# Optimization experiments

Measured on AMD Instinct MI355X. Metric: run time of the kernel, lower is better.

Reference implementation:

```python
import jax, jax.numpy as jnp
import numpy as np

T, B, I, H = 2048, 2048, 1, 20


def setup_inputs() -> dict:
    key = jax.random.key(0)
    k0, k1, k2, k3, k4 = jax.random.split(key, 5)
    x = jax.random.normal(k0, (T, B, I), dtype=jnp.float32)
    # Concatenated gate weights in order [f, i, o, c]; equivalent to the
    # module's 8 separate nn.Linear layers (wf/uf, wi/ui, wo/uo, wc/uc).
    W = jax.random.normal(k1, (4 * H, I), dtype=jnp.float32) * 0.2
    U = jax.random.normal(k2, (4 * H, H), dtype=jnp.float32) * 0.2
    bw = jax.random.normal(k3, (4 * H,), dtype=jnp.float32) * 0.1  # Linear(w*) biases
    bu = jax.random.normal(k4, (4 * H,), dtype=jnp.float32) * 0.1  # Linear(u*) biases
    return {"x": x, "W": W, "U": U, "bw": bw, "bu": bu}


def reference(x, W, U, bw, bu):
    h_dim = U.shape[1]
    b = x.shape[1]
    # Precompute input projections for all timesteps: (T, B, 4H).
    # Original adds both Linear biases (bw from w*, bu from u*) plus zero b*.
    xz = jnp.einsum('tbi,gi->tbg', x, W) + bw + bu

    def step(carry, xz_t):
        h, c = carry
        z = xz_t + h @ U.T  # (B, 4H)
        f, i, o, g = jnp.split(z, 4, axis=-1)
        f = jax.nn.sigmoid(f)
        i = jax.nn.sigmoid(i)
        o = jax.nn.sigmoid(o)
        g = jnp.tanh(g)
        c = f * c + i * g
        h = o * jnp.tanh(c)
        return (h, c), h

    h0 = jnp.zeros((b, h_dim), dtype=x.dtype)
    c0 = jnp.zeros((b, h_dim), dtype=x.dtype)
    (h_last, c_last), h_seq = jax.lax.scan(step, (h0, c0), xz)
    return h_seq, h_last, c_last
```

## Files before the change

### kernel.cpp

```cpp
#include <hip/hip_runtime.h>
#include <cstddef>


constexpr int T = 2048;
constexpr int B = 2048;
constexpr int H = 20;
constexpr int CHUNK = 16;
constexpr int NCH = T / CHUNK;

typedef float f2   __attribute__((ext_vector_type(2)));
typedef float f4ma __attribute__((ext_vector_type(4), may_alias));

__device__ __forceinline__ float rcp_f(float v) { return __builtin_amdgcn_rcpf(v); }
__device__ __forceinline__ float ex2(float v)   { return __builtin_amdgcn_exp2f(v); }
__device__ __forceinline__ float dpp_swap1(float v) {
  return __int_as_float(__builtin_amdgcn_update_dpp(
      0, __float_as_int(v), 0xB1, 0xF, 0xF, true));
}

__global__ __launch_bounds__(64, 1)
void lstm_w8(const float* __restrict__ xg, const float* __restrict__ Wg,
             const float* __restrict__ Ug, const float* __restrict__ bwg,
             const float* __restrict__ bug, float* __restrict__ out) {
  __shared__ float hx[2][64];
  __shared__ float xl[2][CHUNK];

  const int tid = threadIdx.x;
  const int p   = tid & 1;
  const int jr  = tid >> 1;
  const int jc  = (jr < H) ? jr : (H - 1);
  const int b   = blockIdx.x;
  const bool st = (p == 0) && (jr < H);

  constexpr float K1 = 1.44269504f;
  const float s0 = -K1;
  const float s1 = p ? (2.f * K1) : -K1;
  const int g0 = p ? 2 : 0;
  const int g1 = p ? 3 : 1;

  f2 u2[H];
#pragma unroll
  for (int k = 0; k < H; ++k) {
    u2[k].x = Ug[(g0 * H + jc) * H + k] * s0;
    u2[k].y = Ug[(g1 * H + jc) * H + k] * s1;
  }
  f2 w2, b2, A, Bv;
  w2.x = Wg[g0 * H + jc] * s0;  w2.y = Wg[g1 * H + jc] * s1;
  b2.x = (bwg[g0 * H + jc] + bug[g0 * H + jc]) * s0;
  b2.y = (bwg[g1 * H + jc] + bug[g1 * H + jc]) * s1;
  A.x = 1.f;  A.y = p ? -2.f : (2.f * K1);
  Bv.x = 0.f; Bv.y = p ? 1.f : 0.f;

  const int wslot = p ? (32 + jr) : jr;

  for (int q = tid; q < 2 * 64; q += 64) (&hx[0][0])[q] = 0.f;
  if (tid < 2 * CHUNK) (&xl[0][0])[tid] = 0.f;
  __builtin_amdgcn_wave_barrier();

  if (tid < CHUNK) xl[0][tid] = xg[(size_t)tid * B + b];
  float xnext = (tid < CHUNK) ? xg[(size_t)(CHUNK + tid) * B + b] : 0.f;
  __builtin_amdgcn_wave_barrier();

  float c2 = 0.f;
  float hn = 0.f;
  float* outp = out + (size_t)b * H + jc;
  constexpr size_t OS = (size_t)B * H;

  for (int ch = 0; ch < NCH; ++ch) {
    const int cb = ch & 1;
    if (tid < CHUNK) {
      xl[cb ^ 1][tid] = xnext;
      const int tp = (ch + 2) * CHUNK + tid;
      xnext = (tp < T) ? xg[(size_t)tp * B + b] : 0.f;
    }
#pragma unroll
    for (int s = 0; s < CHUNK; ++s) {
      const int P = s & 1;
      __builtin_amdgcn_wave_barrier();
      const f4ma* hp = reinterpret_cast<const f4ma*>(&hx[P][0]);
      const f4ma v0 = hp[0], v1 = hp[1], v2 = hp[2], v3 = hp[3], v4 = hp[4];
      const float xv = xl[cb][s];
      const float hb[H] = {v0.x, v0.y, v0.z, v0.w, v1.x, v1.y, v1.z, v1.w,
                           v2.x, v2.y, v2.z, v2.w, v3.x, v3.y, v3.z, v3.w,
                           v4.x, v4.y, v4.z, v4.w};
      f2 h5;  h5.x  = hb[5];  h5.y  = hb[5];
      f2 h10; h10.x = hb[10]; h10.y = hb[10];
      f2 h15; h15.x = hb[15]; h15.y = hb[15];
      f2 qa = b2, qb = u2[5] * h5, qc = u2[10] * h10, qd = u2[15] * h15;
#pragma unroll
      for (int k = 0; k < 5; ++k)   { f2 hk; hk.x = hb[k]; hk.y = hb[k];
                                      qa = u2[k] * hk + qa; }
#pragma unroll
      for (int k = 6; k < 10; ++k)  { f2 hk; hk.x = hb[k]; hk.y = hb[k];
                                      qb = u2[k] * hk + qb; }
#pragma unroll
      for (int k = 11; k < 15; ++k) { f2 hk; hk.x = hb[k]; hk.y = hb[k];
                                      qc = u2[k] * hk + qc; }
#pragma unroll
      for (int k = 16; k < 20; ++k) { f2 hk; hk.x = hb[k]; hk.y = hb[k];
                                      qd = u2[k] * hk + qd; }
      f2 xv2; xv2.x = xv; xv2.y = xv;
      const f2 z2 = w2 * xv2 + ((qa + qb) + (qc + qd));
      f2 r;
      r.x = rcp_f(1.f + ex2(z2.x));
      r.y = rcp_f(1.f + ex2(z2.y));
      const f2 act2 = A * r + Bv;
      f2 oth;
      oth.x = dpp_swap1(act2.x);
      oth.y = dpp_swap1(act2.y);
      const float fg  = p ? oth.x : act2.x;
      const float og  = p ? act2.x : oth.x;
      const float igt = act2.y * oth.y;
      c2 = fmaf(fg, c2, igt);
      const float r2 = rcp_f(1.f + ex2(c2));
      hn = fmaf(-2.f * og, r2, og);
      hx[P ^ 1][wslot] = hn;
      if (st) *outp = hn;
      outp += OS;
    }
  }

  if (st) {
    out[OS * T + (size_t)b * H + jr] = hn;
    out[OS * (T + 1) + (size_t)b * H + jr] = c2 * 0.34657359f;
  }
}

extern "C" void kernel_launch(void* const* d_in, const int* in_sizes, int n_in,
                              void* d_out, int out_size, void* d_ws, size_t ws_size,
                              hipStream_t stream) {
  (void)in_sizes; (void)n_in; (void)d_ws; (void)ws_size; (void)out_size;
  const float* x  = (const float*)d_in[0];
  const float* W  = (const float*)d_in[1];
  const float* U  = (const float*)d_in[2];
  const float* bw = (const float*)d_in[3];
  const float* bu = (const float*)d_in[4];
  float* out = (float*)d_out;

  lstm_w8<<<dim3(B), dim3(64), 0, stream>>>(x, W, U, bw, bu, out);
}
```

Measured before the change: 530.2 us.

## Process two batch rows per wave and broadcast h via readlane instead of LDS

Each 64-lane wave now runs two independent batch sequences, packing them into the two halves of f2 vectors so the packed FMAs serve two recurrences at once, and launches half as many blocks. The hidden state is no longer exchanged through double-buffered shared memory with wave barriers. Instead each lane pulls h with 20 scalar readlanes per sequence, and x is kept in registers and fetched with readlane. This is meant to cut LDS round-trip latency on the serial critical path and make better use of each wave's ALUs. The cost is 40 readlanes per step, more register pressure, and half the number of waves for latency hiding.

```diff
diff --git a/kernel.cpp b/kernel.cpp
--- a/kernel.cpp
+++ b/kernel.cpp
@@ -8,28 +8,27 @@
 constexpr int CHUNK = 16;
 constexpr int NCH = T / CHUNK;
 
-typedef float f2   __attribute__((ext_vector_type(2)));
-typedef float f4ma __attribute__((ext_vector_type(4), may_alias));
+typedef float f2 __attribute__((ext_vector_type(2)));
 
 __device__ __forceinline__ float rcp_f(float v) { return __builtin_amdgcn_rcpf(v); }
 __device__ __forceinline__ float ex2(float v)   { return __builtin_amdgcn_exp2f(v); }
-__device__ __forceinline__ float dpp_swap1(float v) {
+__device__ __forceinline__ float rdl(float v, int l) {
+  return __int_as_float(__builtin_amdgcn_readlane(__float_as_int(v), l));
+}
+__device__ __forceinline__ float dppswap(float v) {
   return __int_as_float(__builtin_amdgcn_update_dpp(
       0, __float_as_int(v), 0xB1, 0xF, 0xF, true));
 }
 
 __global__ __launch_bounds__(64, 1)
-void lstm_w8(const float* __restrict__ xg, const float* __restrict__ Wg,
+void lstm_rl(const float* __restrict__ xg, const float* __restrict__ Wg,
              const float* __restrict__ Ug, const float* __restrict__ bwg,
              const float* __restrict__ bug, float* __restrict__ out) {
-  __shared__ float hx[2][64];
-  __shared__ float xl[2][CHUNK];
-
   const int tid = threadIdx.x;
   const int p   = tid & 1;
   const int jr  = tid >> 1;
   const int jc  = (jr < H) ? jr : (H - 1);
-  const int b   = blockIdx.x;
+  const int bA  = blockIdx.x * 2;
   const bool st = (p == 0) && (jr < H);
 
   constexpr float K1 = 1.44269504f;
@@ -38,91 +37,104 @@
   const int g0 = p ? 2 : 0;
   const int g1 = p ? 3 : 1;
 
-  f2 u2[H];
+  f2 u0[H], u1[H];
 #pragma unroll
   for (int k = 0; k < H; ++k) {
-    u2[k].x = Ug[(g0 * H + jc) * H + k] * s0;
-    u2[k].y = Ug[(g1 * H + jc) * H + k] * s1;
+    const float a = Ug[(g0 * H + jc) * H + k] * s0;
+    const float b = Ug[(g1 * H + jc) * H + k] * s1;
+    u0[k].x = a; u0[k].y = a;
+    u1[k].x = b; u1[k].y = b;
   }
-  f2 w2, b2, A, Bv;
-  w2.x = Wg[g0 * H + jc] * s0;  w2.y = Wg[g1 * H + jc] * s1;
-  b2.x = (bwg[g0 * H + jc] + bug[g0 * H + jc]) * s0;
-  b2.y = (bwg[g1 * H + jc] + bug[g1 * H + jc]) * s1;
-  A.x = 1.f;  A.y = p ? -2.f : (2.f * K1);
-  Bv.x = 0.f; Bv.y = p ? 1.f : 0.f;
+  f2 w0, w1, bb0, bb1, A1d, B1d;
+  { const float a = Wg[g0 * H + jc] * s0;                 w0.x = a;  w0.y = a;  }
+  { const float a = Wg[g1 * H + jc] * s1;                 w1.x = a;  w1.y = a;  }
+  { const float a = (bwg[g0*H+jc] + bug[g0*H+jc]) * s0;   bb0.x = a; bb0.y = a; }
+  { const float a = (bwg[g1*H+jc] + bug[g1*H+jc]) * s1;   bb1.x = a; bb1.y = a; }
+  { const float a = p ? -2.f : (2.f * K1);                A1d.x = a; A1d.y = a; }
+  { const float a = p ? 1.f : 0.f;                        B1d.x = a; B1d.y = a; }
 
-  const int wslot = p ? (32 + jr) : jr;
+  const int sl = tid & 15;
+  auto ldx = [&](int t) -> f2 {
+    t = (t < T) ? t : (T - 1);
+    return *reinterpret_cast<const f2*>(&xg[(size_t)t * B + bA]);
+  };
+  f2 xc0 = ldx(sl);
+  f2 xc1 = ldx(CHUNK + sl);
 
-  for (int q = tid; q < 2 * 64; q += 64) (&hx[0][0])[q] = 0.f;
-  if (tid < 2 * CHUNK) (&xl[0][0])[tid] = 0.f;
-  __builtin_amdgcn_wave_barrier();
+  f2 c2; c2.x = 0.f; c2.y = 0.f;
+  f2 hn; hn.x = 0.f; hn.y = 0.f;
 
-  if (tid < CHUNK) xl[0][tid] = xg[(size_t)tid * B + b];
-  float xnext = (tid < CHUNK) ? xg[(size_t)(CHUNK + tid) * B + b] : 0.f;
-  __builtin_amdgcn_wave_barrier();
+  constexpr size_t OS = (size_t)B * H;
+  float* outA = out + (size_t)bA * H + jr;
+  float* outB = outA + H;
 
-  float c2 = 0.f;
-  float hn = 0.f;
-  float* outp = out + (size_t)b * H + jc;
-  constexpr size_t OS = (size_t)B * H;
-
-  for (int ch = 0; ch < NCH; ++ch) {
-    const int cb = ch & 1;
-    if (tid < CHUNK) {
-      xl[cb ^ 1][tid] = xnext;
-      const int tp = (ch + 2) * CHUNK + tid;
-      xnext = (tp < T) ? xg[(size_t)tp * B + b] : 0.f;
-    }
-#pragma unroll
-    for (int s = 0; s < CHUNK; ++s) {
-      const int P = s & 1;
-      __builtin_amdgcn_wave_barrier();
-      const f4ma* hp = reinterpret_cast<const f4ma*>(&hx[P][0]);
-      const f4ma v0 = hp[0], v1 = hp[1], v2 = hp[2], v3 = hp[3], v4 = hp[4];
-      const float xv = xl[cb][s];
-      const float hb[H] = {v0.x, v0.y, v0.z, v0.w, v1.x, v1.y, v1.z, v1.w,
-                           v2.x, v2.y, v2.z, v2.w, v3.x, v3.y, v3.z, v3.w,
-                           v4.x, v4.y, v4.z, v4.w};
-      f2 h5;  h5.x  = hb[5];  h5.y  = hb[5];
-      f2 h10; h10.x = hb[10]; h10.y = hb[10];
-      f2 h15; h15.x = hb[15]; h15.y = hb[15];
-      f2 qa = b2, qb = u2[5] * h5, qc = u2[10] * h10, qd = u2[15] * h15;
-#pragma unroll
-      for (int k = 0; k < 5; ++k)   { f2 hk; hk.x = hb[k]; hk.y = hb[k];
-                                      qa = u2[k] * hk + qa; }
-#pragma unroll
-      for (int k = 6; k < 10; ++k)  { f2 hk; hk.x = hb[k]; hk.y = hb[k];
-                                      qb = u2[k] * hk + qb; }
-#pragma unroll
-      for (int k = 11; k < 15; ++k) { f2 hk; hk.x = hb[k]; hk.y = hb[k];
-                                      qc = u2[k] * hk + qc; }
-#pragma unroll
-      for (int k = 16; k < 20; ++k) { f2 hk; hk.x = hb[k]; hk.y = hb[k];
-                                      qd = u2[k] * hk + qd; }
-      f2 xv2; xv2.x = xv; xv2.y = xv;
-      const f2 z2 = w2 * xv2 + ((qa + qb) + (qc + qd));
-      f2 r;
-      r.x = rcp_f(1.f + ex2(z2.x));
-      r.y = rcp_f(1.f + ex2(z2.y));
-      const f2 act2 = A * r + Bv;
-      f2 oth;
-      oth.x = dpp_swap1(act2.x);
-      oth.y = dpp_swap1(act2.y);
-      const float fg  = p ? oth.x : act2.x;
-      const float og  = p ? act2.x : oth.x;
-      const float igt = act2.y * oth.y;
-      c2 = fmaf(fg, c2, igt);
-      const float r2 = rcp_f(1.f + ex2(c2));
-      hn = fmaf(-2.f * og, r2, og);
-      hx[P ^ 1][wslot] = hn;
-      if (st) *outp = hn;
-      outp += OS;
-    }
+#define STEP(SS, XC)                                                         \
+  {                                                                          \
+               \
+    f2 hk[H];                                                                \
+    _Pragma("unroll")                                                        \
+    for (int k = 0; k < H; ++k) {                                            \
+      hk[k].x = rdl(hn.x, 2 * k);                                            \
+      hk[k].y = rdl(hn.y, 2 * k);                                            \
+    }                                                                        \
+    f2 xx;                                                                   \
+    xx.x = rdl(XC.x, (SS));                                                  \
+    xx.y = rdl(XC.y, (SS));                                                  \
+                          \
+    f2 q0a = bb0, q1a = bb1;                                                 \
+    f2 q0b = u0[10] * hk[10], q1b = u1[10] * hk[10];                         \
+    _Pragma("unroll")                                                        \
+    for (int k = 0; k < 10; ++k) {                                           \
+      q0a = u0[k] * hk[k] + q0a;                                             \
+      q1a = u1[k] * hk[k] + q1a;                                             \
+    }                                                                        \
+    _Pragma("unroll")                                                        \
+    for (int k = 11; k < H; ++k) {                                           \
+      q0b = u0[k] * hk[k] + q0b;                                             \
+      q1b = u1[k] * hk[k] + q1b;                                             \
+    }                                                                        \
+    const f2 z0 = w0 * xx + (q0a + q0b);                                     \
+    const f2 z1 = w1 * xx + (q1a + q1b);                                     \
+           \
+    f2 r0, r1;                                                               \
+    r0.x = rcp_f(1.f + ex2(z0.x));  r0.y = rcp_f(1.f + ex2(z0.y));           \
+    r1.x = rcp_f(1.f + ex2(z1.x));  r1.y = rcp_f(1.f + ex2(z1.y));           \
+    const f2 act0 = r0;                                 \
+    const f2 act1 = A1d * r1 + B1d;                \
+    f2 oth0, oth1;                                                           \
+    oth0.x = dppswap(act0.x); oth0.y = dppswap(act0.y);                      \
+    oth1.x = dppswap(act1.x); oth1.y = dppswap(act1.y);                      \
+    f2 fg, og;                                                               \
+    fg.x = p ? oth0.x : act0.x;  fg.y = p ? oth0.y : act0.y;                 \
+    og.x = p ? act0.x : oth0.x;  og.y = p ? act0.y : oth0.y;                 \
+    const f2 igt = act1 * oth1;                  \
+    c2 = fg * c2 + igt;                                                      \
+                           \
+    f2 r2;                                                                   \
+    r2.x = rcp_f(1.f + ex2(c2.x)); r2.y = rcp_f(1.f + ex2(c2.y));            \
+    const f2 tc = r2 * -2.f + 1.f;                                           \
+    hn = og * tc;                                                            \
+    if (st) { *outA = hn.x; *outB = hn.y; }                                  \
+    outA += OS; outB += OS;                                                  \
   }
 
+  for (int ch = 0; ch < NCH; ch += 2) {
+    f2 nx0 = ldx((ch + 2) * CHUNK + sl);
+#pragma unroll
+    for (int s = 0; s < CHUNK; ++s) STEP(s, xc0)
+    xc0 = nx0;
+    f2 nx1 = ldx((ch + 3) * CHUNK + sl);
+#pragma unroll
+    for (int s = 0; s < CHUNK; ++s) STEP(s, xc1)
+    xc1 = nx1;
+  }
+#undef STEP
+
   if (st) {
-    out[OS * T + (size_t)b * H + jr] = hn;
-    out[OS * (T + 1) + (size_t)b * H + jr] = c2 * 0.34657359f;
+    out[OS * T + (size_t)bA * H + jr]           = hn.x;
+    out[OS * T + (size_t)bA * H + H + jr]       = hn.y;
+    out[OS * (T + 1) + (size_t)bA * H + jr]     = c2.x * 0.34657359f;
+    out[OS * (T + 1) + (size_t)bA * H + H + jr] = c2.y * 0.34657359f;
   }
 }
 
@@ -137,5 +149,5 @@
   const float* bu = (const float*)d_in[4];
   float* out = (float*)d_out;
 
-  lstm_w8<<<dim3(B), dim3(64), 0, stream>>>(x, W, U, bw, bu, out);
+  lstm_rl<<<dim3(B / 2), dim3(64), 0, stream>>>(x, W, U, bw, bu, out);
 }
```

After: 584.7 us. +10.3%, slower.
